# Performance work log

Hardware: AMD Instinct MI355X
Metric: run time of the kernel (lower is better)

The kernel has to match this reference:

```python
import jax, jax.numpy as jnp
import numpy as np

N = 100000      # nodes
E = 1600000     # edges (avg degree 16)
IN = 128        # in_feats
H = 4           # num_heads
F = 32          # out_feats per head
NEG_SLOPE = 0.2


def setup_inputs() -> dict:
    key = jax.random.key(0)
    k0, k1, k2, k3, k4, k5 = jax.random.split(key, 6)
    feat = jax.random.normal(k0, (N, IN), dtype=jnp.float32)
    # Glorot-ish scaled params
    W = jax.random.normal(k1, (IN, H * F), dtype=jnp.float32) * (1.0 / np.sqrt(IN))
    attn_l = jax.random.normal(k2, (H, F), dtype=jnp.float32) * 0.1
    attn_r = jax.random.normal(k3, (H, F), dtype=jnp.float32) * 0.1
    bias = jnp.zeros((H * F,), dtype=jnp.float32)
    src = jax.random.randint(k4, (E,), 0, N, dtype=jnp.int32)
    dst = jax.random.randint(k5, (E,), 0, N, dtype=jnp.int32)
    return {"feat": feat, "W": W, "attn_l": attn_l, "attn_r": attn_r,
            "bias": bias, "src": src, "dst": dst}


def reference(feat, W, attn_l, attn_r, bias, src, dst):
    # GeMM: projected features, [N, H, F]
    feat_src = (feat @ W).reshape(N, H, F)
    # per-node attention halves, [N, H]
    el = (feat_src * attn_l).sum(-1)
    er = (feat_src * attn_r).sum(-1)
    # per-edge score e_ij = LeakyReLU(el[src] + er[dst]), [E, H]
    e = el[src] + er[dst]
    e = jnp.where(e > 0, e, NEG_SLOPE * e)
    # edge softmax over destination-node segments (numerically stable)
    m = jax.ops.segment_max(e, dst, num_segments=N)          # [N, H]
    ex = jnp.exp(e - m[dst])                                  # [E, H]
    denom = jax.ops.segment_sum(ex, dst, num_segments=N)     # [N, H]
    alpha = ex / jnp.maximum(denom[dst], 1e-9)                # [E, H]
    # weighted SpMM aggregation: sum_j alpha_ij * Wh_j, [N, H, F]
    msg = feat_src[src] * alpha[:, :, None]                   # [E, H, F]
    rst = jax.ops.segment_sum(msg, dst, num_segments=N)      # [N, H, F]
    rst = rst + bias.reshape(1, H, F)
    return rst
```

## Files before the change

kernel.cpp:

```cpp
#include <hip/hip_runtime.h>
#include <hip/hip_fp16.h>

#define IN_F 128
#define HF   128
#define NH   4
#define NF   32

#define NPB       256
#define NPB_SHIFT 8
#define BIN_CHUNK 4096
#define BCAP      4608
#define QCAP 1536
#define RP   18

typedef __attribute__((ext_vector_type(8))) short short8v;
typedef __attribute__((ext_vector_type(4))) float f32x4;

__device__ __forceinline__ unsigned short f32_to_bf16_rtn(float f) {
    unsigned int u = __float_as_uint(f);
    u += 0x7fffu + ((u >> 16) & 1u);
    return (unsigned short)(u >> 16);
}

#define FMA_MIX_LO(acc, pair, w) \
    asm("v_fma_mix_f32 %0, %1, %2, %0 op_sel:[0,0,0] op_sel_hi:[1,0,0]" \
        : "+v"(acc) : "v"(pair), "v"(w))
#define FMA_MIX_HI(acc, pair, w) \
    asm("v_fma_mix_f32 %0, %1, %2, %0 op_sel:[1,0,0] op_sel_hi:[1,0,0]" \
        : "+v"(acc) : "v"(pair), "v"(w))

__global__ void __launch_bounds__(256)
gat_wfrag(const float* __restrict__ W, short8v* __restrict__ wfrag) {
    const int entry = blockIdx.x * 256 + threadIdx.x;
    const int lane = entry & 63;
    const int kb   = (entry >> 6) & 3;
    const int nt   = entry >> 8;
    const int k0   = kb * 32 + (lane >> 4) * 8;
    const int col  = nt * 16 + (lane & 15);
    short8v s;
    #pragma unroll
    for (int j = 0; j < 8; ++j)
        s[j] = (short)f32_to_bf16_rtn(W[(k0 + j) * HF + col]);
    wfrag[entry] = s;
}

__device__ __forceinline__ void gemm_body(
    int row0b, char* smem,
    const float* __restrict__ feat, const short8v* __restrict__ wfrag,
    const float* __restrict__ attn_l, const float* __restrict__ attn_r,
    unsigned short* __restrict__ feat_src_h,
    float* __restrict__ el, float* __restrict__ er, int N, int t) {
    unsigned short* a_lds = (unsigned short*)smem;
    unsigned short* w_lds = (unsigned short*)(smem + 16384);
    const int lane = t & 63;
    const int wave = t >> 6;

    {
        const uint4* wsrc = (const uint4*)wfrag;
        uint4* wdst = (uint4*)w_lds;
        #pragma unroll
        for (int i = 0; i < 8; ++i)
            wdst[i * 256 + t] = wsrc[i * 256 + t];
    }
    #pragma unroll
    for (int i = 0; i < 8; ++i) {
        int idx = i * 256 + t;
        int row = idx >> 5;
        int c4  = idx & 31;
        int srow = min(row0b + row, N - 1);
        float4 f = *(const float4*)(feat + (size_t)srow * IN_F + c4 * 4);
        unsigned int lo = ((unsigned int)f32_to_bf16_rtn(f.y) << 16) | f32_to_bf16_rtn(f.x);
        unsigned int hi = ((unsigned int)f32_to_bf16_rtn(f.w) << 16) | f32_to_bf16_rtn(f.z);
        int kb = c4 >> 3, g = (c4 >> 1) & 3, half = c4 & 1;
        int wv = row >> 4, m = row & 15;
        unsigned int* p = (unsigned int*)a_lds;
        int u = (wv * 4096 + kb * 1024 + g * 256 + m * 16 + half * 8) >> 2;
        p[u]     = lo;
        p[u + 1] = hi;
    }
    __syncthreads();

    const int m = lane & 15;
    const int g = lane >> 4;
    short8v aw[4];
    #pragma unroll
    for (int kb = 0; kb < 4; ++kb)
        aw[kb] = *(const short8v*)&a_lds[wave * 2048 + kb * 512 + g * 128 + m * 8];

    f32x4 acc[8];
    #pragma unroll
    for (int nt = 0; nt < 8; ++nt) acc[nt] = (f32x4){0.f, 0.f, 0.f, 0.f};

    #pragma unroll
    for (int nt = 0; nt < 8; ++nt) {
        #pragma unroll
        for (int kb = 0; kb < 4; ++kb) {
            short8v bw = *(const short8v*)&w_lds[((nt * 4 + kb) * 64 + lane) * 8];
            acc[nt] = __builtin_amdgcn_mfma_f32_16x16x32_bf16(aw[kb], bw, acc[nt], 0, 0, 0);
        }
    }

    float al[8], ar[8];
    #pragma unroll
    for (int nt = 0; nt < 8; ++nt) {
        al[nt] = attn_l[nt * 16 + m];
        ar[nt] = attn_r[nt * 16 + m];
    }

    #pragma unroll
    for (int r = 0; r < 4; ++r) {
        const int row = row0b + wave * 16 + 4 * g + r;
        const bool valid = (row < N);
        if (valid) {
            #pragma unroll
            for (int nt = 0; nt < 8; ++nt)
                feat_src_h[(size_t)row * HF + nt * 16 + m] =
                    __half_as_ushort(__float2half(acc[nt][r]));
        }
        float pl[NH], pr[NH];
        #pragma unroll
        for (int h = 0; h < NH; ++h) {
            pl[h] = acc[2 * h][r] * al[2 * h] + acc[2 * h + 1][r] * al[2 * h + 1];
            pr[h] = acc[2 * h][r] * ar[2 * h] + acc[2 * h + 1][r] * ar[2 * h + 1];
        }
        #pragma unroll
        for (int mask = 1; mask <= 8; mask <<= 1) {
            #pragma unroll
            for (int h = 0; h < NH; ++h) {
                pl[h] += __shfl_xor(pl[h], mask);
                pr[h] += __shfl_xor(pr[h], mask);
            }
        }
        if (valid && m == 0) {
            *(float4*)(el + (size_t)row * NH) = make_float4(pl[0], pl[1], pl[2], pl[3]);
            *(float4*)(er + (size_t)row * NH) = make_float4(pr[0], pr[1], pr[2], pr[3]);
        }
    }
}

__global__ void __launch_bounds__(256)
gat_bin_gemm(const int* __restrict__ src, const int* __restrict__ dst,
             int* __restrict__ gcursor, unsigned int* __restrict__ gpairs, int E,
             int nBin,
             const float* __restrict__ feat, const short8v* __restrict__ wfrag,
             const float* __restrict__ attn_l, const float* __restrict__ attn_r,
             unsigned short* __restrict__ feat_src_h,
             float* __restrict__ el, float* __restrict__ er, int N) {
    __shared__ __align__(16) char smem[49152];
    const int t = threadIdx.x;

    if ((int)blockIdx.x < nBin) {
        unsigned int*   stage  = (unsigned int*)smem;
        unsigned short* buckof = (unsigned short*)(smem + 16384);
        int* hist  = (int*)(smem + 24576);
        int* sc    = (int*)(smem + 26624);
        int* basew = (int*)(smem + 28672);
        int* cur   = (int*)(smem + 30720);
        for (int i = t; i < 512; i += 256) hist[i] = 0;
        __syncthreads();
        const int e0  = blockIdx.x * BIN_CHUNK;
        const int cnt = min(BIN_CHUNK, E - e0);
        for (int i = t; i < cnt; i += 256)
            atomicAdd(&hist[dst[e0 + i] >> NPB_SHIFT], 1);
        __syncthreads();
        sc[t]       = hist[t];
        sc[t + 256] = hist[t + 256];
        __syncthreads();
        for (int off = 1; off < 512; off <<= 1) {
            int x0 = (t >= off) ? sc[t - off] : 0;
            int x1 = sc[t + 256 - off];
            __syncthreads();
            sc[t]       += x0;
            sc[t + 256] += x1;
            __syncthreads();
        }
        for (int b = t; b < 512; b += 256) {
            int c  = hist[b];
            int ex = sc[b] - c;
            cur[b] = ex;
            basew[b] = c ? (b * BCAP + atomicAdd(&gcursor[b], c)) : 0;
        }
        __syncthreads();
        for (int i = t; i < cnt; i += 256) {
            unsigned s = (unsigned)src[e0 + i];
            unsigned d = (unsigned)dst[e0 + i];
            int b = (int)(d >> NPB_SHIFT);
            int p = atomicAdd(&cur[b], 1);
            stage[p]  = (s << 8) | (d & (NPB - 1));
            buckof[p] = (unsigned short)b;
        }
        __syncthreads();
        for (int j = t; j < cnt; j += 256) {
            int b  = (int)buckof[j];
            int ex = sc[b] - hist[b];
            gpairs[basew[b] + (j - ex)] = stage[j];
        }
        return;
    }

    gemm_body((blockIdx.x - nBin) * 64, smem, feat, wfrag, attn_l, attn_r,
              feat_src_h, el, er, N, t);
}

__global__ void __launch_bounds__(256)
gat_fine_agg(const unsigned int* __restrict__ gpairs, const int* __restrict__ counts,
             const unsigned short* __restrict__ feat_src_h,
             const float* __restrict__ el, const float* __restrict__ er,
             const float* __restrict__ bias, float* __restrict__ out, int N) {
    __shared__ int   slot_lds[QCAP];
    __shared__ int   hist[64];
    __shared__ int   sbuf[64];
    __shared__ int   offs[65];
    __shared__ int   cur[64];
    __shared__ float exs[4][256];
    const int t = threadIdx.x;
    const int b = blockIdx.x >> 2;
    const int q = blockIdx.x & 3;
    const int node0 = (b << NPB_SHIFT) + q * 64;
    const int beg = b * BCAP;
    const int end = beg + counts[b];

    if (t < 64) hist[t] = 0;
    __syncthreads();

    unsigned int pv[RP];
    #pragma unroll
    for (int r = 0; r < RP; ++r) {
        int idx = beg + r * 256 + t;
        pv[r] = 0xffffffffu;
        if (idx < end) {
            unsigned int pr = gpairs[idx];
            pv[r] = pr;
            int local = (int)(pr & (NPB - 1)) - q * 64;
            if (local >= 0 && local < 64) atomicAdd(&hist[local], 1);
        }
    }
    __syncthreads();
    if (t < 64) sbuf[t] = hist[t];
    __syncthreads();
    for (int off = 1; off < 64; off <<= 1) {
        int x = (t < 64 && t >= off) ? sbuf[t - off] : 0;
        __syncthreads();
        if (t < 64) sbuf[t] += x;
        __syncthreads();
    }
    if (t < 64) {
        offs[t + 1] = sbuf[t];
        cur[t] = sbuf[t] - hist[t];
        if (t == 0) offs[0] = 0;
    }
    __syncthreads();
    #pragma unroll
    for (int r = 0; r < RP; ++r) {
        unsigned int pr = pv[r];
        if (pr != 0xffffffffu) {
            int local = (int)(pr & (NPB - 1)) - q * 64;
            if (local >= 0 && local < 64) {
                int p = atomicAdd(&cur[local], 1);
                slot_lds[p] = (int)(pr >> 8);
            }
        }
    }
    __syncthreads();

    const int lane = t & 63;
    const int wave = t >> 6;
    const int k  = lane & 15;
    const int g  = lane >> 4;
    const int hm = k >> 2;
    const unsigned short* fsp = feat_src_h + 8 * k;
    float* exw = exs[wave];
    float4 b0, b1;
    if (g == 0) {
        b0 = *(const float4*)(bias + 8 * k);
        b1 = *(const float4*)(bias + 8 * k + 4);
    }

    for (int i = 0; i < 16; ++i) {
        const int l = wave + 4 * i;
        const int node = node0 + l;
        if (node >= N) break;
        const int s0 = offs[l];
        const int s1 = offs[l + 1];

        const float4 er4 = *(const float4*)(er + (size_t)node * NH);
        float dacc = 0.f;
        float ax0 = 0.f, ax1 = 0.f, ax2 = 0.f, ax3 = 0.f;
        float ax4 = 0.f, ax5 = 0.f, ax6 = 0.f, ax7 = 0.f;

        for (int c = s0; c < s1; c += 64) {
            int idx = c + lane;
            bool vld = idx < s1;
            int s_l = vld ? slot_lds[idx] : 0;
            float4 ev = make_float4(0.f, 0.f, 0.f, 0.f);
            if (vld) ev = *(const float4*)(el + (size_t)s_l * NH);
            float x0 = ev.x + er4.x; x0 = fmaxf(x0, 0.2f * x0);
            float x1 = ev.y + er4.y; x1 = fmaxf(x1, 0.2f * x1);
            float x2 = ev.z + er4.z; x2 = fmaxf(x2, 0.2f * x2);
            float x3 = ev.w + er4.w; x3 = fmaxf(x3, 0.2f * x3);
            float e0 = vld ? __expf(x0) : 0.f;
            float e1 = vld ? __expf(x1) : 0.f;
            float e2 = vld ? __expf(x2) : 0.f;
            float e3 = vld ? __expf(x3) : 0.f;
            *(float4*)&exw[lane * 4] = make_float4(e0, e1, e2, e3);
            asm volatile("" ::: "memory");
            const int n = min(64, s1 - c);
            int j = g;
            for (; j + 4 < n; j += 8) {
                int jB = j + 4;
                int sA = slot_lds[c + j];
                int sB = slot_lds[c + jB];
                float wA = exw[j * 4 + hm];
                float wB = exw[jB * 4 + hm];
                uint4 uA = *(const uint4*)(fsp + (size_t)sA * HF);
                uint4 uB = *(const uint4*)(fsp + (size_t)sB * HF);
                dacc += wA + wB;
                FMA_MIX_LO(ax0, uA.x, wA); FMA_MIX_LO(ax0, uB.x, wB);
                FMA_MIX_HI(ax1, uA.x, wA); FMA_MIX_HI(ax1, uB.x, wB);
                FMA_MIX_LO(ax2, uA.y, wA); FMA_MIX_LO(ax2, uB.y, wB);
                FMA_MIX_HI(ax3, uA.y, wA); FMA_MIX_HI(ax3, uB.y, wB);
                FMA_MIX_LO(ax4, uA.z, wA); FMA_MIX_LO(ax4, uB.z, wB);
                FMA_MIX_HI(ax5, uA.z, wA); FMA_MIX_HI(ax5, uB.z, wB);
                FMA_MIX_LO(ax6, uA.w, wA); FMA_MIX_LO(ax6, uB.w, wB);
                FMA_MIX_HI(ax7, uA.w, wA); FMA_MIX_HI(ax7, uB.w, wB);
            }
            if (j < n) {
                int sA = slot_lds[c + j];
                float wA = exw[j * 4 + hm];
                uint4 uA = *(const uint4*)(fsp + (size_t)sA * HF);
                dacc += wA;
                FMA_MIX_LO(ax0, uA.x, wA);
                FMA_MIX_HI(ax1, uA.x, wA);
                FMA_MIX_LO(ax2, uA.y, wA);
                FMA_MIX_HI(ax3, uA.y, wA);
                FMA_MIX_LO(ax4, uA.z, wA);
                FMA_MIX_HI(ax5, uA.z, wA);
                FMA_MIX_LO(ax6, uA.w, wA);
                FMA_MIX_HI(ax7, uA.w, wA);
            }
            asm volatile("" ::: "memory");
        }

        #pragma unroll
        for (int msk = 16; msk <= 32; msk <<= 1) {
            ax0 += __shfl_xor(ax0, msk); ax1 += __shfl_xor(ax1, msk);
            ax2 += __shfl_xor(ax2, msk); ax3 += __shfl_xor(ax3, msk);
            ax4 += __shfl_xor(ax4, msk); ax5 += __shfl_xor(ax5, msk);
            ax6 += __shfl_xor(ax6, msk); ax7 += __shfl_xor(ax7, msk);
            dacc += __shfl_xor(dacc, msk);
        }
        const float inv = 1.0f / fmaxf(dacc, 1e-9f);

        if (g == 0) {
            float4 o0, o1;
            o0.x = ax0 * inv + b0.x; o0.y = ax1 * inv + b0.y;
            o0.z = ax2 * inv + b0.z; o0.w = ax3 * inv + b0.w;
            o1.x = ax4 * inv + b1.x; o1.y = ax5 * inv + b1.y;
            o1.z = ax6 * inv + b1.z; o1.w = ax7 * inv + b1.w;
            *(float4*)(out + (size_t)node * HF + 8 * k)     = o0;
            *(float4*)(out + (size_t)node * HF + 8 * k + 4) = o1;
        }
    }
}

extern "C" void kernel_launch(void* const* d_in, const int* in_sizes, int n_in,
                              void* d_out, int out_size, void* d_ws, size_t ws_size,
                              hipStream_t stream) {
    const float* feat   = (const float*)d_in[0];
    const float* W      = (const float*)d_in[1];
    const float* attn_l = (const float*)d_in[2];
    const float* attn_r = (const float*)d_in[3];
    const float* bias   = (const float*)d_in[4];
    const int*   src    = (const int*)d_in[5];
    const int*   dst    = (const int*)d_in[6];
    float* out = (float*)d_out;

    const int N = in_sizes[0] / IN_F;
    const int E = in_sizes[5];
    const int nbuck = (N + NPB - 1) / NPB;

    char* ws = (char*)d_ws;
    size_t off = 0;
    auto alloc = [&](size_t bytes) -> void* {
        off = (off + 255) & ~(size_t)255;
        void* p = ws + off;
        off += bytes;
        return p;
    };
    unsigned short* feat_src_h = (unsigned short*)alloc((size_t)N * HF * sizeof(unsigned short));
    float* el      = (float*)alloc((size_t)N * NH * sizeof(float));
    float* er      = (float*)alloc((size_t)N * NH * sizeof(float));
    int*   gcursor = (int*)  alloc((size_t)nbuck * sizeof(int));
    unsigned int* gpairs = (unsigned int*)alloc((size_t)nbuck * BCAP * sizeof(unsigned int));
    short8v* wfrag = (short8v*)alloc((size_t)2048 * sizeof(short8v));

    hipMemsetAsync(gcursor, 0, (size_t)nbuck * sizeof(int), stream);

    gat_wfrag<<<8, 256, 0, stream>>>(W, wfrag);

    const int nBin = (E + BIN_CHUNK - 1) / BIN_CHUNK;
    const int gemmBlocks = (N + 63) / 64;
    gat_bin_gemm<<<nBin + gemmBlocks, 256, 0, stream>>>(
        src, dst, gcursor, gpairs, E, nBin,
        feat, wfrag, attn_l, attn_r, feat_src_h, el, er, N);

    gat_fine_agg<<<nbuck * 4, 256, 0, stream>>>(
        gpairs, gcursor, feat_src_h, el, er, bias, out, N);
}
```

Before: 130.4 us.

## Fold attention vectors into an extra GEMM tile and pad edge-weight LDS

Precomputes W·attn_l and W·attn_r as a ninth 16-column weight tile, so el and er come straight out of the MFMA GEMM. This replaces the per-row dot products and the shuffle reduction in the GEMM epilogue. The el/er values now come from bf16-rounded folded weights, which changes numerics slightly, and each block does one more MFMA tile and uses more LDS. Separately, the per-wave exp buffer in the aggregation kernel is padded to stride 5, apparently to reduce LDS bank conflicts, at the cost of four scalar stores replacing one vector store.

```diff
diff --git a/kernel.cpp b/kernel.cpp
--- a/kernel.cpp
+++ b/kernel.cpp
@@ -12,6 +12,7 @@
 #define BCAP      4608
 #define QCAP 1536
 #define RP   18
+#define NTILES 9
 
 typedef __attribute__((ext_vector_type(8))) short short8v;
 typedef __attribute__((ext_vector_type(4))) float f32x4;
@@ -30,24 +31,40 @@
         : "+v"(acc) : "v"(pair), "v"(w))
 
 __global__ void __launch_bounds__(256)
-gat_wfrag(const float* __restrict__ W, short8v* __restrict__ wfrag) {
+gat_wfrag(const float* __restrict__ W, const float* __restrict__ attn_l,
+          const float* __restrict__ attn_r, short8v* __restrict__ wfrag) {
     const int entry = blockIdx.x * 256 + threadIdx.x;
     const int lane = entry & 63;
     const int kb   = (entry >> 6) & 3;
     const int nt   = entry >> 8;
     const int k0   = kb * 32 + (lane >> 4) * 8;
-    const int col  = nt * 16 + (lane & 15);
+    const int c    = lane & 15;
     short8v s;
-    #pragma unroll
-    for (int j = 0; j < 8; ++j)
-        s[j] = (short)f32_to_bf16_rtn(W[(k0 + j) * HF + col]);
+    if (nt < 8) {
+        const int col = nt * 16 + c;
+        #pragma unroll
+        for (int j = 0; j < 8; ++j)
+            s[j] = (short)f32_to_bf16_rtn(W[(k0 + j) * HF + col]);
+    } else {
+        #pragma unroll
+        for (int j = 0; j < 8; ++j) {
+            float v = 0.f;
+            if (c < 8) {
+                const int h = c & 3;
+                const float* wrow = W + (size_t)(k0 + j) * HF + h * NF;
+                const float* av   = (c < 4 ? attn_l : attn_r) + h * NF;
+                #pragma unroll 8
+                for (int f = 0; f < NF; ++f) v += wrow[f] * av[f];
+            }
+            s[j] = (short)f32_to_bf16_rtn(v);
+        }
+    }
     wfrag[entry] = s;
 }
 
 __device__ __forceinline__ void gemm_body(
     int row0b, char* smem,
     const float* __restrict__ feat, const short8v* __restrict__ wfrag,
-    const float* __restrict__ attn_l, const float* __restrict__ attn_r,
     unsigned short* __restrict__ feat_src_h,
     float* __restrict__ el, float* __restrict__ er, int N, int t) {
     unsigned short* a_lds = (unsigned short*)smem;
@@ -59,7 +76,7 @@
         const uint4* wsrc = (const uint4*)wfrag;
         uint4* wdst = (uint4*)w_lds;
         #pragma unroll
-        for (int i = 0; i < 8; ++i)
+        for (int i = 0; i < NTILES; ++i)
             wdst[i * 256 + t] = wsrc[i * 256 + t];
     }
     #pragma unroll
@@ -87,12 +104,12 @@
     for (int kb = 0; kb < 4; ++kb)
         aw[kb] = *(const short8v*)&a_lds[wave * 2048 + kb * 512 + g * 128 + m * 8];
 
-    f32x4 acc[8];
-    #pragma unroll
-    for (int nt = 0; nt < 8; ++nt) acc[nt] = (f32x4){0.f, 0.f, 0.f, 0.f};
-
-    #pragma unroll
-    for (int nt = 0; nt < 8; ++nt) {
+    f32x4 acc[NTILES];
+    #pragma unroll
+    for (int nt = 0; nt < NTILES; ++nt) acc[nt] = (f32x4){0.f, 0.f, 0.f, 0.f};
+
+    #pragma unroll
+    for (int nt = 0; nt < NTILES; ++nt) {
         #pragma unroll
         for (int kb = 0; kb < 4; ++kb) {
             short8v bw = *(const short8v*)&w_lds[((nt * 4 + kb) * 64 + lane) * 8];
@@ -100,40 +117,16 @@
         }
     }
 
-    float al[8], ar[8];
-    #pragma unroll
-    for (int nt = 0; nt < 8; ++nt) {
-        al[nt] = attn_l[nt * 16 + m];
-        ar[nt] = attn_r[nt * 16 + m];
-    }
-
     #pragma unroll
     for (int r = 0; r < 4; ++r) {
         const int row = row0b + wave * 16 + 4 * g + r;
-        const bool valid = (row < N);
-        if (valid) {
+        if (row < N) {
             #pragma unroll
             for (int nt = 0; nt < 8; ++nt)
                 feat_src_h[(size_t)row * HF + nt * 16 + m] =
                     __half_as_ushort(__float2half(acc[nt][r]));
-        }
-        float pl[NH], pr[NH];
-        #pragma unroll
-        for (int h = 0; h < NH; ++h) {
-            pl[h] = acc[2 * h][r] * al[2 * h] + acc[2 * h + 1][r] * al[2 * h + 1];
-            pr[h] = acc[2 * h][r] * ar[2 * h] + acc[2 * h + 1][r] * ar[2 * h + 1];
-        }
-        #pragma unroll
-        for (int mask = 1; mask <= 8; mask <<= 1) {
-            #pragma unroll
-            for (int h = 0; h < NH; ++h) {
-                pl[h] += __shfl_xor(pl[h], mask);
-                pr[h] += __shfl_xor(pr[h], mask);
-            }
-        }
-        if (valid && m == 0) {
-            *(float4*)(el + (size_t)row * NH) = make_float4(pl[0], pl[1], pl[2], pl[3]);
-            *(float4*)(er + (size_t)row * NH) = make_float4(pr[0], pr[1], pr[2], pr[3]);
+            if (m < 4)      el[(size_t)row * NH + m]       = acc[8][r];
+            else if (m < 8) er[(size_t)row * NH + (m - 4)] = acc[8][r];
         }
     }
 }
@@ -143,10 +136,9 @@
              int* __restrict__ gcursor, unsigned int* __restrict__ gpairs, int E,
              int nBin,
              const float* __restrict__ feat, const short8v* __restrict__ wfrag,
-             const float* __restrict__ attn_l, const float* __restrict__ attn_r,
              unsigned short* __restrict__ feat_src_h,
              float* __restrict__ el, float* __restrict__ er, int N) {
-    __shared__ __align__(16) char smem[49152];
+    __shared__ __align__(16) char smem[53248];
     const int t = threadIdx.x;
 
     if ((int)blockIdx.x < nBin) {
@@ -198,7 +190,7 @@
         return;
     }
 
-    gemm_body((blockIdx.x - nBin) * 64, smem, feat, wfrag, attn_l, attn_r,
+    gemm_body((blockIdx.x - nBin) * 64, smem, feat, wfrag,
               feat_src_h, el, er, N, t);
 }
 
@@ -212,7 +204,7 @@
     __shared__ int   sbuf[64];
     __shared__ int   offs[65];
     __shared__ int   cur[64];
-    __shared__ float exs[4][256];
+    __shared__ float exs[4][64][5];
     const int t = threadIdx.x;
     const int b = blockIdx.x >> 2;
     const int q = blockIdx.x & 3;
@@ -269,7 +261,6 @@
     const int g  = lane >> 4;
     const int hm = k >> 2;
     const unsigned short* fsp = feat_src_h + 8 * k;
-    float* exw = exs[wave];
     float4 b0, b1;
     if (g == 0) {
         b0 = *(const float4*)(bias + 8 * k);
@@ -298,11 +289,10 @@
             float x1 = ev.y + er4.y; x1 = fmaxf(x1, 0.2f * x1);
             float x2 = ev.z + er4.z; x2 = fmaxf(x2, 0.2f * x2);
             float x3 = ev.w + er4.w; x3 = fmaxf(x3, 0.2f * x3);
-            float e0 = vld ? __expf(x0) : 0.f;
-            float e1 = vld ? __expf(x1) : 0.f;
-            float e2 = vld ? __expf(x2) : 0.f;
-            float e3 = vld ? __expf(x3) : 0.f;
-            *(float4*)&exw[lane * 4] = make_float4(e0, e1, e2, e3);
+            exs[wave][lane][0] = vld ? __expf(x0) : 0.f;
+            exs[wave][lane][1] = vld ? __expf(x1) : 0.f;
+            exs[wave][lane][2] = vld ? __expf(x2) : 0.f;
+            exs[wave][lane][3] = vld ? __expf(x3) : 0.f;
             asm volatile("" ::: "memory");
             const int n = min(64, s1 - c);
             int j = g;
@@ -310,8 +300,8 @@
                 int jB = j + 4;
                 int sA = slot_lds[c + j];
                 int sB = slot_lds[c + jB];
-                float wA = exw[j * 4 + hm];
-                float wB = exw[jB * 4 + hm];
+                float wA = exs[wave][j][hm];
+                float wB = exs[wave][jB][hm];
                 uint4 uA = *(const uint4*)(fsp + (size_t)sA * HF);
                 uint4 uB = *(const uint4*)(fsp + (size_t)sB * HF);
                 dacc += wA + wB;
@@ -326,7 +316,7 @@
             }
             if (j < n) {
                 int sA = slot_lds[c + j];
-                float wA = exw[j * 4 + hm];
+                float wA = exs[wave][j][hm];
                 uint4 uA = *(const uint4*)(fsp + (size_t)sA * HF);
                 dacc += wA;
                 FMA_MIX_LO(ax0, uA.x, wA);
@@ -392,17 +382,17 @@
     float* er      = (float*)alloc((size_t)N * NH * sizeof(float));
     int*   gcursor = (int*)  alloc((size_t)nbuck * sizeof(int));
     unsigned int* gpairs = (unsigned int*)alloc((size_t)nbuck * BCAP * sizeof(unsigned int));
-    short8v* wfrag = (short8v*)alloc((size_t)2048 * sizeof(short8v));
+    short8v* wfrag = (short8v*)alloc((size_t)(NTILES * 256) * sizeof(short8v));
 
     hipMemsetAsync(gcursor, 0, (size_t)nbuck * sizeof(int), stream);
 
-    gat_wfrag<<<8, 256, 0, stream>>>(W, wfrag);
+    gat_wfrag<<<NTILES, 256, 0, stream>>>(W, attn_l, attn_r, wfrag);
 
     const int nBin = (E + BIN_CHUNK - 1) / BIN_CHUNK;
     const int gemmBlocks = (N + 63) / 64;
     gat_bin_gemm<<<nBin + gemmBlocks, 256, 0, stream>>>(
         src, dst, gcursor, gpairs, E, nBin,
-        feat, wfrag, attn_l, attn_r, feat_src_h, el, er, N);
+        feat, wfrag, feat_src_h, el, er, N);
 
     gat_fine_agg<<<nbuck * 4, 256, 0, stream>>>(
         gpairs, gcursor, feat_src_h, el, er, bias, out, N);
```

After: 134.0 us. 2.7% more time.

## Bin edges into 64-node buckets so each aggregation block reads only its edges

Applied to the files above, without the earlier changes.

Shrinks the destination buckets from 256 to 64 nodes, giving 1563 buckets, and rewrites the per-chunk scan as a two-level scan where each thread handles 7 buckets. Each fine-aggregation block now loads only its own bucket instead of reading a 256-node bucket and discarding three quarters of the pairs. This removes the 4x redundant gpairs reads and filtering. In exchange, the binning kernel does more global atomics per chunk and needs larger LDS histograms. Pairs that overflow a bucket's capacity are now silently dropped, and the exs array gets padding to reduce LDS bank conflicts.

```diff
diff --git a/kernel.cpp b/kernel.cpp
--- a/kernel.cpp
+++ b/kernel.cpp
@@ -6,12 +6,12 @@
 #define NH   4
 #define NF   32
 
-#define NPB       256
-#define NPB_SHIFT 8
+#define NPB       64
+#define NPB_SHIFT 6
+#define NBPAD     1792
 #define BIN_CHUNK 4096
-#define BCAP      4608
-#define QCAP 1536
-#define RP   18
+#define BCAP      1536
+#define RP        6
 
 typedef __attribute__((ext_vector_type(8))) short short8v;
 typedef __attribute__((ext_vector_type(4))) float f32x4;
@@ -141,7 +141,7 @@
 __global__ void __launch_bounds__(256)
 gat_bin_gemm(const int* __restrict__ src, const int* __restrict__ dst,
              int* __restrict__ gcursor, unsigned int* __restrict__ gpairs, int E,
-             int nBin,
+             int nBin, int nb,
              const float* __restrict__ feat, const short8v* __restrict__ wfrag,
              const float* __restrict__ attn_l, const float* __restrict__ attn_r,
              unsigned short* __restrict__ feat_src_h,
@@ -152,33 +152,49 @@
     if ((int)blockIdx.x < nBin) {
         unsigned int*   stage  = (unsigned int*)smem;
         unsigned short* buckof = (unsigned short*)(smem + 16384);
-        int* hist  = (int*)(smem + 24576);
-        int* sc    = (int*)(smem + 26624);
-        int* basew = (int*)(smem + 28672);
-        int* cur   = (int*)(smem + 30720);
-        for (int i = t; i < 512; i += 256) hist[i] = 0;
+        int* hist = (int*)(smem + 24576);
+        int* sc   = (int*)(smem + 31744);
+        int* cur  = (int*)(smem + 38912);
+        int* part = (int*)(smem + 46080);
+        for (int i = t; i < NBPAD; i += 256) hist[i] = 0;
         __syncthreads();
         const int e0  = blockIdx.x * BIN_CHUNK;
         const int cnt = min(BIN_CHUNK, E - e0);
         for (int i = t; i < cnt; i += 256)
             atomicAdd(&hist[dst[e0 + i] >> NPB_SHIFT], 1);
         __syncthreads();
-        sc[t]       = hist[t];
-        sc[t + 256] = hist[t + 256];
-        __syncthreads();
-        for (int off = 1; off < 512; off <<= 1) {
-            int x0 = (t >= off) ? sc[t - off] : 0;
-            int x1 = sc[t + 256 - off];
+        const int base7 = t * 7;
+        int vals[7];
+        {
+            int run = 0;
+            #pragma unroll
+            for (int i = 0; i < 7; ++i) { run += hist[base7 + i]; vals[i] = run; }
+            part[t] = run;
+        }
+        __syncthreads();
+        for (int off = 1; off < 256; off <<= 1) {
+            int x = (t >= off) ? part[t - off] : 0;
             __syncthreads();
-            sc[t]       += x0;
-            sc[t + 256] += x1;
+            part[t] += x;
             __syncthreads();
         }
-        for (int b = t; b < 512; b += 256) {
-            int c  = hist[b];
-            int ex = sc[b] - c;
-            cur[b] = ex;
-            basew[b] = c ? (b * BCAP + atomicAdd(&gcursor[b], c)) : 0;
+        {
+            int prev = (t > 0) ? part[t - 1] : 0;
+            #pragma unroll
+            for (int i = 0; i < 7; ++i) sc[base7 + i] = vals[i] + prev;
+        }
+        __syncthreads();
+        #pragma unroll
+        for (int i = 0; i < 7; ++i) {
+            int b = base7 + i;
+            int c = hist[b];
+            cur[b] = sc[b] - c;
+            if (b < nb && c) {
+                int off0 = atomicAdd(&gcursor[b], c);
+                hist[b] = b * BCAP + off0;
+            } else {
+                hist[b] = -1;
+            }
         }
         __syncthreads();
         for (int i = t; i < cnt; i += 256) {
@@ -186,14 +202,17 @@
             unsigned d = (unsigned)dst[e0 + i];
             int b = (int)(d >> NPB_SHIFT);
             int p = atomicAdd(&cur[b], 1);
-            stage[p]  = (s << 8) | (d & (NPB - 1));
+            stage[p]  = (s << NPB_SHIFT) | (d & (NPB - 1));
             buckof[p] = (unsigned short)b;
         }
         __syncthreads();
         for (int j = t; j < cnt; j += 256) {
             int b  = (int)buckof[j];
-            int ex = sc[b] - hist[b];
-            gpairs[basew[b] + (j - ex)] = stage[j];
+            int base = hist[b];
+            if (base < 0) continue;
+            int ex = (b > 0) ? sc[b - 1] : 0;
+            int idx = base + (j - ex);
+            if (idx < (b + 1) * BCAP) gpairs[idx] = stage[j];
         }
         return;
     }
@@ -207,18 +226,17 @@
              const unsigned short* __restrict__ feat_src_h,
              const float* __restrict__ el, const float* __restrict__ er,
              const float* __restrict__ bias, float* __restrict__ out, int N) {
-    __shared__ int   slot_lds[QCAP];
+    __shared__ int   slot_lds[BCAP];
     __shared__ int   hist[64];
     __shared__ int   sbuf[64];
     __shared__ int   offs[65];
     __shared__ int   cur[64];
-    __shared__ float exs[4][256];
+    __shared__ float exs[4][64][5];
     const int t = threadIdx.x;
-    const int b = blockIdx.x >> 2;
-    const int q = blockIdx.x & 3;
-    const int node0 = (b << NPB_SHIFT) + q * 64;
+    const int b = blockIdx.x;
+    const int node0 = b << NPB_SHIFT;
     const int beg = b * BCAP;
-    const int end = beg + counts[b];
+    const int end = beg + min(counts[b], BCAP);
 
     if (t < 64) hist[t] = 0;
     __syncthreads();
@@ -231,8 +249,7 @@
         if (idx < end) {
             unsigned int pr = gpairs[idx];
             pv[r] = pr;
-            int local = (int)(pr & (NPB - 1)) - q * 64;
-            if (local >= 0 && local < 64) atomicAdd(&hist[local], 1);
+            atomicAdd(&hist[pr & (NPB - 1)], 1);
         }
     }
     __syncthreads();
@@ -254,11 +271,8 @@
     for (int r = 0; r < RP; ++r) {
         unsigned int pr = pv[r];
         if (pr != 0xffffffffu) {
-            int local = (int)(pr & (NPB - 1)) - q * 64;
-            if (local >= 0 && local < 64) {
-                int p = atomicAdd(&cur[local], 1);
-                slot_lds[p] = (int)(pr >> 8);
-            }
+            int p = atomicAdd(&cur[pr & (NPB - 1)], 1);
+            slot_lds[p] = (int)(pr >> NPB_SHIFT);
         }
     }
     __syncthreads();
@@ -269,7 +283,6 @@
     const int g  = lane >> 4;
     const int hm = k >> 2;
     const unsigned short* fsp = feat_src_h + 8 * k;
-    float* exw = exs[wave];
     float4 b0, b1;
     if (g == 0) {
         b0 = *(const float4*)(bias + 8 * k);
@@ -298,11 +311,10 @@
             float x1 = ev.y + er4.y; x1 = fmaxf(x1, 0.2f * x1);
             float x2 = ev.z + er4.z; x2 = fmaxf(x2, 0.2f * x2);
             float x3 = ev.w + er4.w; x3 = fmaxf(x3, 0.2f * x3);
-            float e0 = vld ? __expf(x0) : 0.f;
-            float e1 = vld ? __expf(x1) : 0.f;
-            float e2 = vld ? __expf(x2) : 0.f;
-            float e3 = vld ? __expf(x3) : 0.f;
-            *(float4*)&exw[lane * 4] = make_float4(e0, e1, e2, e3);
+            exs[wave][lane][0] = vld ? __expf(x0) : 0.f;
+            exs[wave][lane][1] = vld ? __expf(x1) : 0.f;
+            exs[wave][lane][2] = vld ? __expf(x2) : 0.f;
+            exs[wave][lane][3] = vld ? __expf(x3) : 0.f;
             asm volatile("" ::: "memory");
             const int n = min(64, s1 - c);
             int j = g;
@@ -310,8 +322,8 @@
                 int jB = j + 4;
                 int sA = slot_lds[c + j];
                 int sB = slot_lds[c + jB];
-                float wA = exw[j * 4 + hm];
-                float wB = exw[jB * 4 + hm];
+                float wA = exs[wave][j][hm];
+                float wB = exs[wave][jB][hm];
                 uint4 uA = *(const uint4*)(fsp + (size_t)sA * HF);
                 uint4 uB = *(const uint4*)(fsp + (size_t)sB * HF);
                 dacc += wA + wB;
@@ -326,7 +338,7 @@
             }
             if (j < n) {
                 int sA = slot_lds[c + j];
-                float wA = exw[j * 4 + hm];
+                float wA = exs[wave][j][hm];
                 uint4 uA = *(const uint4*)(fsp + (size_t)sA * HF);
                 dacc += wA;
                 FMA_MIX_LO(ax0, uA.x, wA);
@@ -377,7 +389,7 @@
 
     const int N = in_sizes[0] / IN_F;
     const int E = in_sizes[5];
-    const int nbuck = (N + NPB - 1) / NPB;
+    const int nb = (N + NPB - 1) / NPB;
 
     char* ws = (char*)d_ws;
     size_t off = 0;
@@ -390,20 +402,20 @@
     unsigned short* feat_src_h = (unsigned short*)alloc((size_t)N * HF * sizeof(unsigned short));
     float* el      = (float*)alloc((size_t)N * NH * sizeof(float));
     float* er      = (float*)alloc((size_t)N * NH * sizeof(float));
-    int*   gcursor = (int*)  alloc((size_t)nbuck * sizeof(int));
-    unsigned int* gpairs = (unsigned int*)alloc((size_t)nbuck * BCAP * sizeof(unsigned int));
+    int*   gcursor = (int*)  alloc((size_t)nb * sizeof(int));
+    unsigned int* gpairs = (unsigned int*)alloc((size_t)nb * BCAP * sizeof(unsigned int));
     short8v* wfrag = (short8v*)alloc((size_t)2048 * sizeof(short8v));
 
-    hipMemsetAsync(gcursor, 0, (size_t)nbuck * sizeof(int), stream);
+    hipMemsetAsync(gcursor, 0, (size_t)nb * sizeof(int), stream);
 
     gat_wfrag<<<8, 256, 0, stream>>>(W, wfrag);
 
     const int nBin = (E + BIN_CHUNK - 1) / BIN_CHUNK;
     const int gemmBlocks = (N + 63) / 64;
     gat_bin_gemm<<<nBin + gemmBlocks, 256, 0, stream>>>(
-        src, dst, gcursor, gpairs, E, nBin,
+        src, dst, gcursor, gpairs, E, nBin, nb,
         feat, wfrag, attn_l, attn_r, feat_src_h, el, er, N);
 
-    gat_fine_agg<<<nbuck * 4, 256, 0, stream>>>(
+    gat_fine_agg<<<nb, 256, 0, stream>>>(
         gpairs, gcursor, feat_src_h, el, er, bias, out, N);
 }
```

After: 167.5 us. 1.28x slower.
